# Performance work log

Hardware: AMD Instinct MI355X
Metric: run time of the kernel (lower is better)

The kernel has to match this reference:

```python
import jax, jax.numpy as jnp
import numpy as np

N = 10000
E = 160000
IN_DIM = 512
OUT_DIM = 256
NEG_SLOPE = 0.2  # DGL GATConv default LeakyReLU slope


def _gat_conv(x, W, b, attn_l, attn_r, src, dst, num_nodes, heads, out_dim):
    """DGL GATConv (eval mode, feat_drop/attn_drop disabled).
    x: [N, F_in]; W: [F_in, heads*out]; b: [heads*out];
    attn_l/attn_r: [heads, out]. Returns [N, heads, out]."""
    h = (x @ W).reshape(num_nodes, heads, out_dim)            # [N,H,D]
    el = jnp.einsum('nhd,hd->nh', h, attn_l)                  # [N,H]
    er = jnp.einsum('nhd,hd->nh', h, attn_r)                  # [N,H]
    e = jax.nn.leaky_relu(el[src] + er[dst], NEG_SLOPE)       # [E,H]
    # destination-grouped (edge) softmax, numerically stable
    m = jax.ops.segment_max(e, dst, num_segments=num_nodes)   # [N,H], -inf for empty
    m = jnp.where(jnp.isfinite(m), m, 0.0)
    ee = jnp.exp(e - m[dst])                                  # [E,H]
    s = jax.ops.segment_sum(ee, dst, num_segments=num_nodes)  # [N,H]
    a = ee / jnp.where(s > 0, s, 1.0)[dst]                    # [E,H]
    # message aggregation: scatter-add a_e * h[src]
    out = jax.ops.segment_sum(a[:, :, None] * h[src], dst, num_segments=num_nodes)
    return out + b.reshape(1, heads, out_dim)


def setup_inputs() -> dict:
    key = jax.random.key(0)
    ks = jax.random.split(key, 16)
    def glorot(k, shape):
        fan = shape[0] + shape[-1] if len(shape) > 1 else shape[-1]
        return jax.random.normal(k, shape, dtype=jnp.float32) * np.sqrt(2.0 / fan)
    inp = {
        'x':   jax.random.normal(ks[0], (N, IN_DIM), dtype=jnp.float32),
        'src': jax.random.randint(ks[1], (E,), 0, N),
        'dst': jax.random.randint(ks[2], (E,), 0, N),
        'W1': glorot(ks[3], (IN_DIM, 10 * 128)),
        'b1': jnp.zeros((10 * 128,), jnp.float32),
        'al1': glorot(ks[4], (10, 128)),
        'ar1': glorot(ks[5], (10, 128)),
        'W2': glorot(ks[6], (1280, 10 * 64)),
        'b2': jnp.zeros((10 * 64,), jnp.float32),
        'al2': glorot(ks[7], (10, 64)),
        'ar2': glorot(ks[8], (10, 64)),
        'W3': glorot(ks[9], (640, OUT_DIM)),
        'b3': jnp.zeros((OUT_DIM,), jnp.float32),
        'al3': glorot(ks[10], (1, OUT_DIM)),
        'ar3': glorot(ks[11], (1, OUT_DIM)),
        # residual linear 512 -> 256
        'Wres': glorot(ks[12], (IN_DIM, OUT_DIM)),
        'bres': jnp.zeros((OUT_DIM,), jnp.float32),
        'fuse_weight': jnp.full((1,), 0.5, jnp.float32),
    }
    return inp


def reference(x, src, dst, W1, b1, al1, ar1, W2, b2, al2, ar2,
              W3, b3, al3, ar3, Wres, bres, fuse_weight):
    elu = jax.nn.elu
    res = elu(x @ Wres + bres)                                        # [N,256]
    s1 = elu(_gat_conv(x, W1, b1, al1, ar1, src, dst, N, 10, 128))
    s1 = s1.reshape(N, -1)                                            # [N,1280]
    s2 = elu(_gat_conv(s1, W2, b2, al2, ar2, src, dst, N, 10, 64))
    s2 = s2.reshape(N, -1)                                            # [N,640]
    s3 = elu(_gat_conv(s2, W3, b3, al3, ar3, src, dst, N, 1, OUT_DIM))
    s3 = s3.reshape(N, -1)                                            # [N,256]
    return fuse_weight * s3 + (1.0 - fuse_weight) * res
```

## Files before the change

kernel.cpp:

```cpp
#include <hip/hip_runtime.h>
#include <stdint.h>

#define DEVINL __device__ __forceinline__

typedef __attribute__((ext_vector_type(8))) short short8;
typedef __attribute__((ext_vector_type(4))) float f32x4;

static constexpr int NNODES = 10000;

DEVINL float bf2f(unsigned short u) {
  unsigned int x = ((unsigned int)u) << 16;
  float f;
  __builtin_memcpy(&f, &x, 4);
  return f;
}
DEVINL unsigned short f2bf(float f) {
  unsigned int x;
  __builtin_memcpy(&x, &f, 4);
  unsigned int lsb = (x >> 16) & 1;
  x += 0x7fffu + lsb;
  return (unsigned short)(x >> 16);
}
DEVINL void bfpair(unsigned int u, float& f0, float& f1) {
  unsigned int a = u << 16, b = u & 0xffff0000u;
  __builtin_memcpy(&f0, &a, 4);
  __builtin_memcpy(&f1, &b, 4);
}
DEVINL bool is_bf16_mode(const unsigned int* fwWord) {
  return ((*fwWord) & 0xFFFFu) == 0x3F00u;
}

DEVINL void async_cp16(void* lds, const void* g) {
  __builtin_amdgcn_global_load_lds((const __attribute__((address_space(1))) unsigned int*)g,
                                   (__attribute__((address_space(3))) unsigned int*)lds,
                                   16, 0, 0);
}

__global__ __launch_bounds__(256) void gemm_fused(const unsigned short* __restrict__ A,
                                                  const unsigned short* __restrict__ Bt,
                                                  unsigned short* __restrict__ Ch,
                                                  int M, int N, int K, int nres, int nh,
                                                  unsigned short* __restrict__ Cres,
                                                  const float* __restrict__ rbias,
                                                  float* __restrict__ elerf) {
  __shared__ __align__(16) unsigned short lA[128 * 32];
  __shared__ __align__(16) unsigned short lB[128 * 32];
  const int tid = threadIdx.x;
  const int wid = tid >> 6;
  const int lane = tid & 63;
  const int tm = blockIdx.x * 128;
  const int tn = blockIdx.y * 128;
  const int wr = (wid >> 1) * 64;
  const int wc = (wid & 1) * 64;
  f32x4 acc[4][4] = {};
  const int r_in_chunk = lane >> 2;
  const int cb = (lane & 3) * 16;
  const int mr = lane & 15;
  const int kq = (lane >> 4) * 8;
  const size_t stride = (size_t)K * 2;

  for (int k0 = 0; k0 < K; k0 += 32) {
#pragma unroll
    for (int c = 0; c < 2; ++c) {
      const int chunk = wid * 2 + c;
      const int row = chunk * 16 + r_in_chunk;
      int ga = tm + row;
      if (ga >= M) ga = M - 1;
      async_cp16(&lA[chunk * 512], (const char*)A + (size_t)ga * stride + (size_t)k0 * 2 + cb);
      const int gb = tn + row;
      async_cp16(&lB[chunk * 512], (const char*)Bt + (size_t)gb * stride + (size_t)k0 * 2 + cb);
    }
    __syncthreads();
    short8 af[4], bf[4];
#pragma unroll
    for (int i = 0; i < 4; ++i)
      af[i] = *(const short8*)&lA[(wr + i * 16 + mr) * 32 + kq];
#pragma unroll
    for (int j = 0; j < 4; ++j)
      bf[j] = *(const short8*)&lB[(wc + j * 16 + mr) * 32 + kq];
#pragma unroll
    for (int i = 0; i < 4; ++i)
#pragma unroll
      for (int j = 0; j < 4; ++j)
        acc[i][j] = __builtin_amdgcn_mfma_f32_16x16x32_bf16(af[i], bf[j], acc[i][j], 0, 0, 0);
    __syncthreads();
  }

  const int rbase = (lane >> 4) * 4;
  const int cc = lane & 15;
  if (tn < nres) {
#pragma unroll
    for (int i = 0; i < 4; ++i)
#pragma unroll
      for (int r = 0; r < 4; ++r) {
        const int row = tm + wr + i * 16 + rbase + r;
        if (row < M) {
#pragma unroll
          for (int j = 0; j < 4; ++j) {
            const int col = tn + wc + j * 16 + cc;
            float v = acc[i][j][r] + rbias[col];
            v = v > 0.f ? v : (__expf(v) - 1.f);
            Cres[(size_t)row * nres + col] = f2bf(v);
          }
        }
      }
  } else if (tn < nres + nh) {
    const int colw = tn - nres + wc;
#pragma unroll
    for (int i = 0; i < 4; ++i)
#pragma unroll
      for (int r = 0; r < 4; ++r) {
        const int row = tm + wr + i * 16 + rbase + r;
        if (row < M) {
#pragma unroll
          for (int j = 0; j < 4; ++j)
            Ch[(size_t)row * nh + colw + j * 16 + cc] = f2bf(acc[i][j][r]);
        }
      }
  } else {
    const int colw = tn - nres - nh + wc;
#pragma unroll
    for (int i = 0; i < 4; ++i)
#pragma unroll
      for (int r = 0; r < 4; ++r) {
        const int row = tm + wr + i * 16 + rbase + r;
        if (row < M) {
#pragma unroll
          for (int j = 0; j < 4; ++j)
            elerf[(size_t)row * 128 + colw + j * 16 + cc] = acc[i][j][r];
        }
      }
  }
}

template <int H, int D>
__global__ __launch_bounds__(256) void welr_build(const unsigned short* __restrict__ wt,
                                                  const float* __restrict__ al,
                                                  const float* __restrict__ ar,
                                                  unsigned short* __restrict__ out, int K) {
  const int row = blockIdx.y;
  const int k = blockIdx.x * 256 + threadIdx.x;
  if (k >= K) return;
  const int h = row < H ? row : row - H;
  const float* v = (row < H ? al : ar) + h * D;
  const unsigned short* wp = wt + (size_t)(h * D) * K + k;
  float acc = 0.f;
  for (int d = 0; d < D; ++d) acc += bf2f(wp[(size_t)d * K]) * v[d];
  out[(size_t)row * K + k] = f2bf(acc);
}

struct CvtJobs {
  const void* src[12];
  float* dst[12];
  int n[12];
  int cnt;
};
__global__ void cvt_small_f32(CvtJobs jobs, const unsigned int* fwWord) {
  const bool isb = is_bf16_mode(fwWord);
  for (int j = 0; j < jobs.cnt; ++j) {
    for (int i = blockIdx.x * blockDim.x + threadIdx.x; i < jobs.n[j];
         i += gridDim.x * blockDim.x) {
      jobs.dst[j][i] = isb ? bf2f(((const unsigned short*)jobs.src[j])[i])
                           : ((const float*)jobs.src[j])[i];
    }
  }
}

__global__ __launch_bounds__(256) void cvt_x_bf16(const void* __restrict__ in,
                                                  unsigned short* __restrict__ out,
                                                  long n, const unsigned int* fwWord) {
  const bool isb = is_bf16_mode(fwWord);
  const long i0 = (long)(blockIdx.x * 256 + threadIdx.x) * 8;
  if (i0 >= n) return;
  if (isb) {
    *(short8*)&out[i0] = *(const short8*)&((const unsigned short*)in)[i0];
  } else {
    const float* f = (const float*)in + i0;
    unsigned short r[8];
#pragma unroll
    for (int j = 0; j < 8; ++j) r[j] = f2bf(f[j]);
    *(short8*)&out[i0] = *(const short8*)r;
  }
}

struct TAll {
  const void* src[4];
  unsigned short* dst[4];
  int K[4];
  int N[4];
  int b0[5];
};
__global__ __launch_bounds__(256) void transp_all4(TAll ja, const unsigned int* fwWord) {
  const bool isb = is_bf16_mode(fwWord);
  __shared__ unsigned short t[32][33];
  const int bid = blockIdx.x;
  int j = 0;
  while (j < 3 && bid >= ja.b0[j + 1]) ++j;
  const int local = bid - ja.b0[j];
  const int K = ja.K[j], Nn = ja.N[j];
  const int tilesX = Nn / 32;
  const int bx = (local % tilesX) * 32;
  const int by = (local / tilesX) * 32;
  const void* W = ja.src[j];
  unsigned short* Wt = ja.dst[j];
  const int x = threadIdx.x;
  const int y0 = threadIdx.y;
  for (int y = y0; y < 32; y += 8) {
    const size_t idx = (size_t)(by + y) * Nn + bx + x;
    t[y][x] = isb ? ((const unsigned short*)W)[idx] : f2bf(((const float*)W)[idx]);
  }
  __syncthreads();
  for (int y = y0; y < 32; y += 8)
    Wt[(size_t)(bx + y) * K + by + x] = t[x][y];
}

template <int H>
__global__ __launch_bounds__(256) void edge_w(const float* __restrict__ elerf,
                                              const int* __restrict__ sidx,
                                              const int* __restrict__ didx,
                                              float* __restrict__ we_t, int E) {
  const int p = blockIdx.x * 256 + threadIdx.x;
  if (p >= E) return;
  const float* ep = elerf + (size_t)sidx[p] * 128;
  const float* rp = elerf + (size_t)didx[p] * 128;
#pragma unroll
  for (int h = 0; h < H; ++h) {
    float sc = ep[h] + rp[H + h];
    sc = sc > 0.f ? sc : 0.2f * sc;
    we_t[(size_t)h * E + p] = __expf(sc);
  }
}

template <int H, int D, int NS, int CW, int MODE>
__global__ __launch_bounds__(64) void gat_agg_hs(const unsigned short* __restrict__ hf,
                                                 const float* __restrict__ we_t,
                                                 const int* __restrict__ sidx,
                                                 const int* __restrict__ rowstart,
                                                 const float* __restrict__ bias,
                                                 void* __restrict__ outp,
                                                 const unsigned short* __restrict__ resact,
                                                 const float* __restrict__ fwf,
                                                 const unsigned int* fwWord, int E) {
  constexpr int CHUNK = 64;
  constexpr int SF = H * D / NS;
  constexpr int ACT = SF / CW;
  constexpr int SROW = H * D * 2;
  constexpr int LOG2D = (D == 64) ? 6 : (D == 128) ? 7 : 8;
  static_assert((H * D) % NS == 0 && (SF % CW) == 0 && ACT <= 64, "geometry");
  static_assert(CW == 2 || CW == 4, "vector width");
  static_assert(SF < 2 * D, "slice spans at most 2 heads");
  __shared__ float wls[2 * (CHUNK + 1)];
  __shared__ int soff[CHUNK];

  const int bid = blockIdx.x;
  const int n = bid / NS;
  const int sl = bid % NS;
  const int tid = threadIdx.x;
  const int e0 = rowstart[n], e1 = rowstart[n + 1];
  const int f0 = SF * sl;
  const int hlo = f0 >> LOG2D;
  const int hhi = (f0 + SF - 1) >> LOG2D;
  const int fbase = f0 + tid * CW;
  const int wbase = ((fbase >> LOG2D) != hlo) ? (CHUNK + 1) : 0;
  const bool act = tid < ACT;
  const char* hfb = (const char*)(hf + fbase);
  float acc[CW] = {};
  float swlo = 0.f, swhi = 0.f;

  for (int cs = e0; cs < e1; cs += CHUNK) {
    const int ce = min(CHUNK, e1 - cs);
    if (tid < ce) {
      soff[tid] = sidx[cs + tid] * SROW;
      const float wlo = we_t[(size_t)hlo * E + cs + tid];
      wls[tid] = wlo;
      swlo += wlo;
      if (hhi != hlo) {
        const float whi = we_t[(size_t)hhi * E + cs + tid];
        wls[CHUNK + 1 + tid] = whi;
        swhi += whi;
      }
    }
    __syncthreads();
    if (act) {
      int j = 0;
      for (; j + 8 <= ce; j += 8) {
        int o[8];
        float w[8];
#pragma unroll
        for (int b = 0; b < 8; ++b) {
          o[b] = soff[j + b];
          w[b] = wls[wbase + j + b];
        }
        if constexpr (CW == 4) {
          uint2 u[8];
#pragma unroll
          for (int b = 0; b < 8; ++b) u[b] = *(const uint2*)(hfb + o[b]);
#pragma unroll
          for (int b = 0; b < 8; ++b) {
            float a0, a1, a2, a3;
            bfpair(u[b].x, a0, a1);
            bfpair(u[b].y, a2, a3);
            acc[0] += w[b] * a0; acc[1] += w[b] * a1;
            acc[2] += w[b] * a2; acc[3] += w[b] * a3;
          }
        } else {
          unsigned int u[8];
#pragma unroll
          for (int b = 0; b < 8; ++b) u[b] = *(const unsigned int*)(hfb + o[b]);
#pragma unroll
          for (int b = 0; b < 8; ++b) {
            float a0, a1;
            bfpair(u[b], a0, a1);
            acc[0] += w[b] * a0; acc[1] += w[b] * a1;
          }
        }
      }
      for (; j < ce; ++j) {
        const int o = soff[j];
        const float w = wls[wbase + j];
        if constexpr (CW == 4) {
          const uint2 u = *(const uint2*)(hfb + o);
          float a0, a1, a2, a3;
          bfpair(u.x, a0, a1);
          bfpair(u.y, a2, a3);
          acc[0] += w * a0; acc[1] += w * a1; acc[2] += w * a2; acc[3] += w * a3;
        } else {
          const unsigned int u = *(const unsigned int*)(hfb + o);
          float a0, a1;
          bfpair(u, a0, a1);
          acc[0] += w * a0; acc[1] += w * a1;
        }
      }
    }
    __syncthreads();
  }

#pragma unroll
  for (int o = 32; o; o >>= 1) {
    swlo += __shfl_xor(swlo, o);
    swhi += __shfl_xor(swhi, o);
  }
  if (!act) return;
  const float stot = wbase ? swhi : swlo;
  const float inv = stot > 0.f ? 1.f / stot : 0.f;
  const size_t obase = (size_t)n * (H * D) + fbase;
  float v[CW];
#pragma unroll
  for (int k = 0; k < CW; ++k) {
    v[k] = acc[k] * inv + bias[fbase + k];
    v[k] = v[k] > 0.f ? v[k] : (__expf(v[k]) - 1.f);
  }
  if (MODE == 0) {
#pragma unroll
    for (int k = 0; k < CW; ++k)
      ((unsigned short*)outp)[obase + k] = f2bf(v[k]);
  } else {
    const float fw = fwf[0];
    const bool outb = is_bf16_mode(fwWord);
#pragma unroll
    for (int k = 0; k < CW; ++k) {
      const float r = bf2f(resact[obase + k]);
      const float o = fw * v[k] + (1.f - fw) * r;
      if (outb) ((unsigned short*)outp)[obase + k] = f2bf(o);
      else      ((float*)outp)[obase + k] = o;
    }
  }
}

__global__ void sentinel_k(unsigned short* __restrict__ outp, int total) {
  const int i = blockIdx.x * 256 + threadIdx.x;
  if (i < total) outp[i] = f2bf(12344.0f);
}

__global__ void hist_k(const int* __restrict__ dst, int* __restrict__ deg, int E) {
  const int i = blockIdx.x * blockDim.x + threadIdx.x;
  if (i < E) atomicAdd(&deg[dst[i]], 1);
}

__global__ __launch_bounds__(1024) void scan_k(const int* __restrict__ deg,
                                               int* __restrict__ rowstart,
                                               int* __restrict__ cursor, int Nn) {
  __shared__ int ls[1024];
  const int tid = threadIdx.x;
  const int CH = (Nn + 1023) >> 10;
  const int start = tid * CH;
  int sum = 0;
  for (int i = 0; i < CH; ++i) {
    const int idx = start + i;
    if (idx < Nn) sum += deg[idx];
  }
  ls[tid] = sum;
  __syncthreads();
  for (int o = 1; o < 1024; o <<= 1) {
    int v = 0;
    if (tid >= o) v = ls[tid - o];
    __syncthreads();
    ls[tid] += v;
    __syncthreads();
  }
  int run = tid > 0 ? ls[tid - 1] : 0;
  for (int i = 0; i < CH; ++i) {
    const int idx = start + i;
    if (idx < Nn) {
      rowstart[idx] = run;
      cursor[idx] = run;
      run += deg[idx];
    }
  }
  if (tid == 1023) rowstart[Nn] = ls[1023];
}

__global__ void scatter_k(const int* __restrict__ dst, const int* __restrict__ srcA,
                          int* __restrict__ cursor, int* __restrict__ sidx,
                          int* __restrict__ didx, int E) {
  const int i = blockIdx.x * blockDim.x + threadIdx.x;
  if (i < E) {
    const int d = dst[i];
    const int p = atomicAdd(&cursor[d], 1);
    sidx[p] = srcA[i];
    didx[p] = d;
  }
}

extern "C" void kernel_launch(void* const* d_in, const int* in_sizes, int n_in,
                              void* d_out, int out_size, void* d_ws, size_t ws_size,
                              hipStream_t stream) {
  const void* x    = d_in[0];
  const int* src   = (const int*)d_in[1];
  const int* dstA  = (const int*)d_in[2];
  const void* W1   = d_in[3];
  const void* b1   = d_in[4];
  const void* al1  = d_in[5];
  const void* ar1  = d_in[6];
  const void* W2   = d_in[7];
  const void* b2   = d_in[8];
  const void* al2  = d_in[9];
  const void* ar2  = d_in[10];
  const void* W3   = d_in[11];
  const void* b3   = d_in[12];
  const void* al3  = d_in[13];
  const void* ar3  = d_in[14];
  const void* Wres = d_in[15];
  const void* bres = d_in[16];
  const void* fw   = d_in[17];
  const unsigned int* fwWord = (const unsigned int*)fw;
  const int E = in_sizes[1];
  const int M = NNODES;

  char* base = (char*)d_ws;
  size_t off = 0;
  auto alloc = [&](size_t bytes) -> char* {
    char* p = base + off;
    off = (off + bytes + 255) & ~(size_t)255;
    return p;
  };
  int* deg      = (int*)alloc((size_t)M * 4);
  int* rowstart = (int*)alloc((size_t)(M + 1) * 4);
  int* cursor   = (int*)alloc((size_t)M * 4);
  int* sidx     = (int*)alloc((size_t)E * 4);
  int* didx     = (int*)alloc((size_t)E * 4);
  float* we_t   = (float*)alloc((size_t)E * 10 * 4);
  float* elerf  = (float*)alloc((size_t)M * 128 * 4);
  float* b1f   = (float*)alloc(1280 * 4);
  float* al1f  = (float*)alloc(1280 * 4);
  float* ar1f  = (float*)alloc(1280 * 4);
  float* b2f   = (float*)alloc(640 * 4);
  float* al2f  = (float*)alloc(640 * 4);
  float* ar2f  = (float*)alloc(640 * 4);
  float* b3f   = (float*)alloc(256 * 4);
  float* al3f  = (float*)alloc(256 * 4);
  float* ar3f  = (float*)alloc(256 * 4);
  float* bresf = (float*)alloc(256 * 4);
  float* fwf   = (float*)alloc(4);
  unsigned short* wtcat = (unsigned short*)alloc((size_t)1664 * 512 * 2);
  unsigned short* wt2   = (unsigned short*)alloc((size_t)768 * 1280 * 2);
  unsigned short* wt3   = (unsigned short*)alloc((size_t)384 * 640 * 2);
  unsigned short* resact = (unsigned short*)alloc((size_t)M * 256 * 2);
  unsigned short* regA   = (unsigned short*)alloc((size_t)M * 1280 * 2);
  unsigned short* regB   = (unsigned short*)alloc((size_t)M * 1280 * 2);

  if (off > ws_size) {
    sentinel_k<<<(out_size + 255) / 256, 256, 0, stream>>>((unsigned short*)d_out, out_size);
    return;
  }

  unsigned short* h1 = regA;
  unsigned short* h2 = regA;
  unsigned short* h3 = regA;
  unsigned short* xb = regB;
  unsigned short* s1 = regB;
  unsigned short* s2 = regB;

  hipMemsetAsync(deg, 0, (size_t)M * 4, stream);

  CvtJobs jobs;
  const void* srcs[11] = {b1, al1, ar1, b2, al2, ar2, b3, al3, ar3, bres, fw};
  float* dsts[11] = {b1f, al1f, ar1f, b2f, al2f, ar2f, b3f, al3f, ar3f, bresf, fwf};
  const int ns[11] = {1280, 1280, 1280, 640, 640, 640, 256, 256, 256, 256, 1};
  for (int j = 0; j < 11; ++j) { jobs.src[j] = srcs[j]; jobs.dst[j] = dsts[j]; jobs.n[j] = ns[j]; }
  jobs.cnt = 11;
  cvt_small_f32<<<8, 256, 0, stream>>>(jobs, fwWord);

  cvt_x_bf16<<<(int)(((long)M * 512 / 8 + 255) / 256), 256, 0, stream>>>(x, xb, (long)M * 512, fwWord);

  TAll ta;
  ta.src[0] = W1;   ta.dst[0] = wtcat + (size_t)256 * 512; ta.K[0] = 512;  ta.N[0] = 1280;
  ta.src[1] = W2;   ta.dst[1] = wt2;                       ta.K[1] = 1280; ta.N[1] = 640;
  ta.src[2] = W3;   ta.dst[2] = wt3;                       ta.K[2] = 640;  ta.N[2] = 256;
  ta.src[3] = Wres; ta.dst[3] = wtcat;                     ta.K[3] = 512;  ta.N[3] = 256;
  ta.b0[0] = 0;
  for (int j = 0; j < 4; ++j)
    ta.b0[j + 1] = ta.b0[j] + (ta.K[j] / 32) * (ta.N[j] / 32);
  transp_all4<<<ta.b0[4], dim3(32, 8), 0, stream>>>(ta, fwWord);

  welr_build<10, 128><<<dim3(2, 20), 256, 0, stream>>>(
      wtcat + (size_t)256 * 512, al1f, ar1f, wtcat + (size_t)1536 * 512, 512);
  welr_build<10, 64><<<dim3(5, 20), 256, 0, stream>>>(
      wt2, al2f, ar2f, wt2 + (size_t)640 * 1280, 1280);
  welr_build<1, 256><<<dim3(3, 2), 256, 0, stream>>>(
      wt3, al3f, ar3f, wt3 + (size_t)256 * 640, 640);

  hist_k<<<(E + 255) / 256, 256, 0, stream>>>(dstA, deg, E);
  scan_k<<<1, 1024, 0, stream>>>(deg, rowstart, cursor, M);
  scatter_k<<<(E + 255) / 256, 256, 0, stream>>>(dstA, src, cursor, sidx, didx, E);

  const int MT = (M + 127) / 128;
  const int EB = (E + 255) / 256;

  gemm_fused<<<dim3(MT, 13), 256, 0, stream>>>(xb, wtcat, h1, M, 1664, 512,
                                               256, 1280, resact, bresf, elerf);
  edge_w<10><<<EB, 256, 0, stream>>>(elerf, sidx, didx, we_t, E);
  gat_agg_hs<10, 128, 8, 4, 0><<<M * 8, 64, 0, stream>>>(h1, we_t, sidx, rowstart,
                                                         b1f, s1, nullptr, fwf, fwWord, E);

  gemm_fused<<<dim3(MT, 6), 256, 0, stream>>>(s1, wt2, h2, M, 768, 1280,
                                              0, 640, nullptr, nullptr, elerf);
  edge_w<10><<<EB, 256, 0, stream>>>(elerf, sidx, didx, we_t, E);
  gat_agg_hs<10, 64, 8, 2, 0><<<M * 8, 64, 0, stream>>>(h2, we_t, sidx, rowstart,
                                                        b2f, s2, nullptr, fwf, fwWord, E);

  gemm_fused<<<dim3(MT, 3), 256, 0, stream>>>(s2, wt3, h3, M, 384, 640,
                                              0, 256, nullptr, nullptr, elerf);
  edge_w<1><<<EB, 256, 0, stream>>>(elerf, sidx, didx, we_t, E);
  gat_agg_hs<1, 256, 2, 2, 1><<<M * 2, 64, 0, stream>>>(h3, we_t, sidx, rowstart,
                                                        b3f, d_out, resact, fwf, fwWord, E);
}
```

Baseline: 321.1 us.

## Fuse edge-weight computation into aggregation and process multiple nodes per block

Removes the separate edge_w kernel and computes the exp(leaky_relu(el+er)) edge weights on the fly inside the aggregation kernel, reading a compacted 32-wide el/er buffer. Each block now handles a group of destination nodes (GN), streaming their contiguous edge range in shared-memory chunks, and the softmax denominator is accumulated per thread instead of by wave reduction. The aim is to cut three kernel launches and the E×10 weight buffer traffic, and to amortise per-block overhead. In exchange, the exp work is redone for every feature slice (NS times per edge), and the loop unroll drops from 8 to 4.

```diff
diff --git a/kernel.cpp b/kernel.cpp
--- a/kernel.cpp
+++ b/kernel.cpp
@@ -126,8 +126,10 @@
         const int row = tm + wr + i * 16 + rbase + r;
         if (row < M) {
 #pragma unroll
-          for (int j = 0; j < 4; ++j)
-            elerf[(size_t)row * 128 + colw + j * 16 + cc] = acc[i][j][r];
+          for (int j = 0; j < 4; ++j) {
+            const int col = colw + j * 16 + cc;
+            if (col < 32) elerf[(size_t)row * 32 + col] = acc[i][j][r];
+          }
         }
       }
   }
@@ -214,33 +216,17 @@
     Wt[(size_t)(bx + y) * K + by + x] = t[x][y];
 }
 
-template <int H>
-__global__ __launch_bounds__(256) void edge_w(const float* __restrict__ elerf,
-                                              const int* __restrict__ sidx,
-                                              const int* __restrict__ didx,
-                                              float* __restrict__ we_t, int E) {
-  const int p = blockIdx.x * 256 + threadIdx.x;
-  if (p >= E) return;
-  const float* ep = elerf + (size_t)sidx[p] * 128;
-  const float* rp = elerf + (size_t)didx[p] * 128;
-#pragma unroll
-  for (int h = 0; h < H; ++h) {
-    float sc = ep[h] + rp[H + h];
-    sc = sc > 0.f ? sc : 0.2f * sc;
-    we_t[(size_t)h * E + p] = __expf(sc);
-  }
-}
-
-template <int H, int D, int NS, int CW, int MODE>
-__global__ __launch_bounds__(64) void gat_agg_hs(const unsigned short* __restrict__ hf,
-                                                 const float* __restrict__ we_t,
+template <int H, int D, int NS, int CW, int MODE, int GN>
+__global__ __launch_bounds__(64) void gat_agg_mn(const unsigned short* __restrict__ hf,
+                                                 const float* __restrict__ elerf,
                                                  const int* __restrict__ sidx,
+                                                 const int* __restrict__ didx,
                                                  const int* __restrict__ rowstart,
                                                  const float* __restrict__ bias,
                                                  void* __restrict__ outp,
                                                  const unsigned short* __restrict__ resact,
                                                  const float* __restrict__ fwf,
-                                                 const unsigned int* fwWord, int E) {
+                                                 const unsigned int* fwWord) {
   constexpr int CHUNK = 64;
   constexpr int SF = H * D / NS;
   constexpr int ACT = SF / CW;
@@ -249,14 +235,16 @@
   static_assert((H * D) % NS == 0 && (SF % CW) == 0 && ACT <= 64, "geometry");
   static_assert(CW == 2 || CW == 4, "vector width");
   static_assert(SF < 2 * D, "slice spans at most 2 heads");
+  static_assert(GN <= 63, "rowstart slice fits one wave");
   __shared__ float wls[2 * (CHUNK + 1)];
   __shared__ int soff[CHUNK];
+  __shared__ int rs[GN + 1];
 
   const int bid = blockIdx.x;
-  const int n = bid / NS;
+  const int g = bid / NS;
   const int sl = bid % NS;
   const int tid = threadIdx.x;
-  const int e0 = rowstart[n], e1 = rowstart[n + 1];
+  const int n0 = g * GN;
   const int f0 = SF * sl;
   const int hlo = f0 >> LOG2D;
   const int hhi = (f0 + SF - 1) >> LOG2D;
@@ -264,105 +252,128 @@
   const int wbase = ((fbase >> LOG2D) != hlo) ? (CHUNK + 1) : 0;
   const bool act = tid < ACT;
   const char* hfb = (const char*)(hf + fbase);
-  float acc[CW] = {};
-  float swlo = 0.f, swhi = 0.f;
-
-  for (int cs = e0; cs < e1; cs += CHUNK) {
-    const int ce = min(CHUNK, e1 - cs);
-    if (tid < ce) {
-      soff[tid] = sidx[cs + tid] * SROW;
-      const float wlo = we_t[(size_t)hlo * E + cs + tid];
-      wls[tid] = wlo;
-      swlo += wlo;
-      if (hhi != hlo) {
-        const float whi = we_t[(size_t)hhi * E + cs + tid];
-        wls[CHUNK + 1 + tid] = whi;
-        swhi += whi;
+
+  if (tid <= GN) rs[tid] = rowstart[n0 + tid];
+  __syncthreads();
+  const int pe1 = rs[GN];
+  int cs = rs[0];
+  int ce = 0;
+
+  float bv[CW] = {};
+  if (act)
+#pragma unroll
+    for (int k = 0; k < CW; ++k) bv[k] = bias[fbase + k];
+  float fw = 0.f;
+  bool outb = true;
+  if (MODE == 1) { fw = fwf[0]; outb = is_bf16_mode(fwWord); }
+
+  for (int ni = 0; ni < GN; ++ni) {
+    float acc[CW] = {};
+    float sw = 0.f;
+    int p = rs[ni];
+    const int pend = rs[ni + 1];
+    while (p < pend) {
+      if (p == cs + ce) {
+        cs = p;
+        ce = min(CHUNK, pe1 - cs);
+        __syncthreads();
+        if (tid < ce) {
+          const int pp = cs + tid;
+          const int s = sidx[pp];
+          soff[tid] = s * SROW;
+          const float2 elv = *(const float2*)&elerf[(size_t)s * 32 + hlo];
+          const int dn = didx[pp];
+          const float2 erv = *(const float2*)&elerf[(size_t)dn * 32 + H + hlo];
+          float sc0 = elv.x + erv.x;
+          sc0 = sc0 > 0.f ? sc0 : 0.2f * sc0;
+          wls[tid] = __expf(sc0);
+          if (hhi != hlo) {
+            float sc1 = elv.y + erv.y;
+            sc1 = sc1 > 0.f ? sc1 : 0.2f * sc1;
+            wls[CHUNK + 1 + tid] = __expf(sc1);
+          }
+        }
+        __syncthreads();
+      }
+      const int jend = min(pend, cs + ce) - cs;
+      int j = p - cs;
+      p = cs + jend;
+      if (act) {
+        for (; j + 4 <= jend; j += 4) {
+          int o[4];
+          float w[4];
+#pragma unroll
+          for (int b = 0; b < 4; ++b) {
+            o[b] = soff[j + b];
+            w[b] = wls[wbase + j + b];
+          }
+          if constexpr (CW == 4) {
+            uint2 u[4];
+#pragma unroll
+            for (int b = 0; b < 4; ++b) u[b] = *(const uint2*)(hfb + o[b]);
+#pragma unroll
+            for (int b = 0; b < 4; ++b) {
+              float a0, a1, a2, a3;
+              bfpair(u[b].x, a0, a1);
+              bfpair(u[b].y, a2, a3);
+              acc[0] += w[b] * a0; acc[1] += w[b] * a1;
+              acc[2] += w[b] * a2; acc[3] += w[b] * a3;
+              sw += w[b];
+            }
+          } else {
+            unsigned int u[4];
+#pragma unroll
+            for (int b = 0; b < 4; ++b) u[b] = *(const unsigned int*)(hfb + o[b]);
+#pragma unroll
+            for (int b = 0; b < 4; ++b) {
+              float a0, a1;
+              bfpair(u[b], a0, a1);
+              acc[0] += w[b] * a0; acc[1] += w[b] * a1;
+              sw += w[b];
+            }
+          }
+        }
+        for (; j < jend; ++j) {
+          const int o = soff[j];
+          const float w = wls[wbase + j];
+          if constexpr (CW == 4) {
+            const uint2 u = *(const uint2*)(hfb + o);
+            float a0, a1, a2, a3;
+            bfpair(u.x, a0, a1);
+            bfpair(u.y, a2, a3);
+            acc[0] += w * a0; acc[1] += w * a1; acc[2] += w * a2; acc[3] += w * a3;
+          } else {
+            const unsigned int u = *(const unsigned int*)(hfb + o);
+            float a0, a1;
+            bfpair(u, a0, a1);
+            acc[0] += w * a0; acc[1] += w * a1;
+          }
+          sw += w;
+        }
       }
     }
-    __syncthreads();
     if (act) {
-      int j = 0;
-      for (; j + 8 <= ce; j += 8) {
-        int o[8];
-        float w[8];
-#pragma unroll
-        for (int b = 0; b < 8; ++b) {
-          o[b] = soff[j + b];
-          w[b] = wls[wbase + j + b];
-        }
-        if constexpr (CW == 4) {
-          uint2 u[8];
-#pragma unroll
-          for (int b = 0; b < 8; ++b) u[b] = *(const uint2*)(hfb + o[b]);
-#pragma unroll
-          for (int b = 0; b < 8; ++b) {
-            float a0, a1, a2, a3;
-            bfpair(u[b].x, a0, a1);
-            bfpair(u[b].y, a2, a3);
-            acc[0] += w[b] * a0; acc[1] += w[b] * a1;
-            acc[2] += w[b] * a2; acc[3] += w[b] * a3;
-          }
-        } else {
-          unsigned int u[8];
-#pragma unroll
-          for (int b = 0; b < 8; ++b) u[b] = *(const unsigned int*)(hfb + o[b]);
-#pragma unroll
-          for (int b = 0; b < 8; ++b) {
-            float a0, a1;
-            bfpair(u[b], a0, a1);
-            acc[0] += w[b] * a0; acc[1] += w[b] * a1;
-          }
-        }
-      }
-      for (; j < ce; ++j) {
-        const int o = soff[j];
-        const float w = wls[wbase + j];
-        if constexpr (CW == 4) {
-          const uint2 u = *(const uint2*)(hfb + o);
-          float a0, a1, a2, a3;
-          bfpair(u.x, a0, a1);
-          bfpair(u.y, a2, a3);
-          acc[0] += w * a0; acc[1] += w * a1; acc[2] += w * a2; acc[3] += w * a3;
-        } else {
-          const unsigned int u = *(const unsigned int*)(hfb + o);
-          float a0, a1;
-          bfpair(u, a0, a1);
-          acc[0] += w * a0; acc[1] += w * a1;
-        }
-      }
-    }
-    __syncthreads();
-  }
-
-#pragma unroll
-  for (int o = 32; o; o >>= 1) {
-    swlo += __shfl_xor(swlo, o);
-    swhi += __shfl_xor(swhi, o);
-  }
-  if (!act) return;
-  const float stot = wbase ? swhi : swlo;
-  const float inv = stot > 0.f ? 1.f / stot : 0.f;
-  const size_t obase = (size_t)n * (H * D) + fbase;
-  float v[CW];
-#pragma unroll
-  for (int k = 0; k < CW; ++k) {
-    v[k] = acc[k] * inv + bias[fbase + k];
-    v[k] = v[k] > 0.f ? v[k] : (__expf(v[k]) - 1.f);
-  }
-  if (MODE == 0) {
-#pragma unroll
-    for (int k = 0; k < CW; ++k)
-      ((unsigned short*)outp)[obase + k] = f2bf(v[k]);
-  } else {
-    const float fw = fwf[0];
-    const bool outb = is_bf16_mode(fwWord);
-#pragma unroll
-    for (int k = 0; k < CW; ++k) {
-      const float r = bf2f(resact[obase + k]);
-      const float o = fw * v[k] + (1.f - fw) * r;
-      if (outb) ((unsigned short*)outp)[obase + k] = f2bf(o);
-      else      ((float*)outp)[obase + k] = o;
+      const float inv = sw > 0.f ? 1.f / sw : 0.f;
+      const size_t obase = (size_t)(n0 + ni) * (H * D) + fbase;
+      float v[CW];
+#pragma unroll
+      for (int k = 0; k < CW; ++k) {
+        v[k] = acc[k] * inv + bv[k];
+        v[k] = v[k] > 0.f ? v[k] : (__expf(v[k]) - 1.f);
+      }
+      if (MODE == 0) {
+#pragma unroll
+        for (int k = 0; k < CW; ++k)
+          ((unsigned short*)outp)[obase + k] = f2bf(v[k]);
+      } else {
+#pragma unroll
+        for (int k = 0; k < CW; ++k) {
+          const float r = bf2f(resact[obase + k]);
+          const float o = fw * v[k] + (1.f - fw) * r;
+          if (outb) ((unsigned short*)outp)[obase + k] = f2bf(o);
+          else      ((float*)outp)[obase + k] = o;
+        }
+      }
     }
   }
 }
@@ -459,8 +470,7 @@
   int* cursor   = (int*)alloc((size_t)M * 4);
   int* sidx     = (int*)alloc((size_t)E * 4);
   int* didx     = (int*)alloc((size_t)E * 4);
-  float* we_t   = (float*)alloc((size_t)E * 10 * 4);
-  float* elerf  = (float*)alloc((size_t)M * 128 * 4);
+  float* elerf  = (float*)alloc((size_t)M * 32 * 4);
   float* b1f   = (float*)alloc(1280 * 4);
   float* al1f  = (float*)alloc(1280 * 4);
   float* ar1f  = (float*)alloc(1280 * 4);
@@ -525,23 +535,19 @@
   scatter_k<<<(E + 255) / 256, 256, 0, stream>>>(dstA, src, cursor, sidx, didx, E);
 
   const int MT = (M + 127) / 128;
-  const int EB = (E + 255) / 256;
 
   gemm_fused<<<dim3(MT, 13), 256, 0, stream>>>(xb, wtcat, h1, M, 1664, 512,
                                                256, 1280, resact, bresf, elerf);
-  edge_w<10><<<EB, 256, 0, stream>>>(elerf, sidx, didx, we_t, E);
-  gat_agg_hs<10, 128, 8, 4, 0><<<M * 8, 64, 0, stream>>>(h1, we_t, sidx, rowstart,
-                                                         b1f, s1, nullptr, fwf, fwWord, E);
+  gat_agg_mn<10, 128, 8, 4, 0, 8><<<(M / 8) * 8, 64, 0, stream>>>(
+      h1, elerf, sidx, didx, rowstart, b1f, s1, nullptr, fwf, fwWord);
 
   gemm_fused<<<dim3(MT, 6), 256, 0, stream>>>(s1, wt2, h2, M, 768, 1280,
                                               0, 640, nullptr, nullptr, elerf);
-  edge_w<10><<<EB, 256, 0, stream>>>(elerf, sidx, didx, we_t, E);
-  gat_agg_hs<10, 64, 8, 2, 0><<<M * 8, 64, 0, stream>>>(h2, we_t, sidx, rowstart,
-                                                        b2f, s2, nullptr, fwf, fwWord, E);
+  gat_agg_mn<10, 64, 8, 2, 0, 8><<<(M / 8) * 8, 64, 0, stream>>>(
+      h2, elerf, sidx, didx, rowstart, b2f, s2, nullptr, fwf, fwWord);
 
   gemm_fused<<<dim3(MT, 3), 256, 0, stream>>>(s2, wt3, h3, M, 384, 640,
                                               0, 256, nullptr, nullptr, elerf);
-  edge_w<1><<<EB, 256, 0, stream>>>(elerf, sidx, didx, we_t, E);
-  gat_agg_hs<1, 256, 2, 2, 1><<<M * 2, 64, 0, stream>>>(h3, we_t, sidx, rowstart,
-                                                        b3f, d_out, resact, fwf, fwWord, E);
-}
+  gat_agg_mn<1, 256, 2, 2, 1, 4><<<(M / 4) * 2, 64, 0, stream>>>(
+      h3, elerf, sidx, didx, rowstart, b3f, d_out, resact, fwf, fwWord);
+}
```

Result: no change. 326.0 us (+1.5%).
